# Kernel optimization log

Measured on AMD Instinct MI355X. Metric: run time of the kernel, lower is better.

Reference implementation:

```python
import jax, jax.numpy as jnp
import numpy as np

N_NODES = 100000
N_EDGES = 800000
D = 64      # conv_dim == out_dim (skip connection)
H = 128     # conv hidden width


def _w(k, i, o):
    return jax.random.normal(k, (i, o), jnp.float32) * (1.0 / np.sqrt(i))


def setup_inputs() -> dict:
    key = jax.random.key(0)
    ks = jax.random.split(key, 40)
    inp = {
        "edge_feat": jax.random.normal(ks[0], (N_EDGES, D), jnp.float32),
        "node_feat": jax.random.normal(ks[1], (N_NODES, D), jnp.float32),
        "graph_attr": jax.random.normal(ks[2], (1, D), jnp.float32),
        "src": jax.random.randint(ks[3], (N_EDGES,), 0, N_NODES),
        "dst": jax.random.randint(ks[4], (N_EDGES,), 0, N_NODES),
        # pre-dense MLPs (dims=[64,64], Softplus, activate_last)
        "pre_edge_w": _w(ks[5], D, D), "pre_edge_b": jnp.zeros((D,), jnp.float32),
        "pre_node_w": _w(ks[6], D, D), "pre_node_b": jnp.zeros((D,), jnp.float32),
        "pre_attr_w": _w(ks[7], D, D), "pre_attr_b": jnp.zeros((D,), jnp.float32),
        # conv edge MLP: [4D, H, H, D]
        "edge_w0": _w(ks[8], 4 * D, H), "edge_b0": jnp.zeros((H,), jnp.float32),
        "edge_w1": _w(ks[9], H, H),     "edge_b1": jnp.zeros((H,), jnp.float32),
        "edge_w2": _w(ks[10], H, D),    "edge_b2": jnp.zeros((D,), jnp.float32),
        # conv node MLP: [3D, H, H, D]
        "node_w0": _w(ks[11], 3 * D, H), "node_b0": jnp.zeros((H,), jnp.float32),
        "node_w1": _w(ks[12], H, H),     "node_b1": jnp.zeros((H,), jnp.float32),
        "node_w2": _w(ks[13], H, D),     "node_b2": jnp.zeros((D,), jnp.float32),
        # conv attr MLP: [3D, H, H, D]
        "attr_w0": _w(ks[14], 3 * D, H), "attr_b0": jnp.zeros((H,), jnp.float32),
        "attr_w1": _w(ks[15], H, H),     "attr_b1": jnp.zeros((H,), jnp.float32),
        "attr_w2": _w(ks[16], H, D),     "attr_b2": jnp.zeros((D,), jnp.float32),
    }
    return inp


def _mlp(x, layers):
    # Linear + Softplus after every layer (activate_last=True)
    for w, b in layers:
        x = jax.nn.softplus(x @ w + b)
    return x


def reference(edge_feat, node_feat, graph_attr, src, dst,
              pre_edge_w, pre_edge_b, pre_node_w, pre_node_b, pre_attr_w, pre_attr_b,
              edge_w0, edge_b0, edge_w1, edge_b1, edge_w2, edge_b2,
              node_w0, node_b0, node_w1, node_b1, node_w2, node_b2,
              attr_w0, attr_b0, attr_w1, attr_b1, attr_w2, attr_b2):
    e_in, v_in, u_in = edge_feat, node_feat, graph_attr

    # pre-dense MLPs
    e = _mlp(edge_feat, [(pre_edge_w, pre_edge_b)])   # [E, D]
    v = _mlp(node_feat, [(pre_node_w, pre_node_b)])   # [N, D]
    u = _mlp(graph_attr, [(pre_attr_w, pre_attr_b)])  # [1, D]

    n_nodes = v.shape[0]

    # edge update: hstack([v_src, v_dst, e, u_broadcast]) -> edge MLP
    edge_in = jnp.concatenate(
        [v[src], v[dst], e, jnp.broadcast_to(u, (e.shape[0], u.shape[1]))], axis=1)  # [E, 4D]
    e_new = _mlp(edge_in, [(edge_w0, edge_b0), (edge_w1, edge_b1), (edge_w2, edge_b2)])  # [E, D]

    # node update: mean of incoming edge messages (segment-mean over dst)
    cnt = jax.ops.segment_sum(jnp.ones((e_new.shape[0], 1), e_new.dtype), dst,
                              num_segments=n_nodes)
    ve = jax.ops.segment_sum(e_new, dst, num_segments=n_nodes) / jnp.maximum(cnt, 1.0)
    node_in = jnp.concatenate(
        [v, ve, jnp.broadcast_to(u, (n_nodes, u.shape[1]))], axis=1)  # [N, 3D]
    v_new = _mlp(node_in, [(node_w0, node_b0), (node_w1, node_b1), (node_w2, node_b2)])  # [N, D]

    # attr update: mean readouts over edges and nodes
    ue = jnp.mean(e_new, axis=0, keepdims=True)  # [1, D]
    uv = jnp.mean(v_new, axis=0, keepdims=True)  # [1, D]
    attr_in = jnp.concatenate([u, ue, uv], axis=1)  # [1, 3D]
    u_new = _mlp(attr_in, [(attr_w0, attr_b0), (attr_w1, attr_b1), (attr_w2, attr_b2)])  # [1, D]

    # skip connections
    return (e_new + e_in, v_new + v_in, u_new + u_in)
```

## Files before the change

### kernel.cpp

```cpp
#include <hip/hip_runtime.h>
#include <cstddef>


typedef __attribute__((ext_vector_type(8))) short short8;
typedef __attribute__((ext_vector_type(4))) float f32x4;
typedef __attribute__((ext_vector_type(4))) unsigned int u32x4;
typedef __attribute__((ext_vector_type(2))) unsigned int u32x2;

__device__ __forceinline__ float sp(float x) {
    return fmaxf(x, 0.f) + __logf(1.f + __expf(-fabsf(x)));
}
__device__ __forceinline__ unsigned short f2bf(float x) {
    unsigned int u = __float_as_uint(x);
    u += 0x7fff + ((u >> 16) & 1);
    return (unsigned short)(u >> 16);
}
__device__ __forceinline__ unsigned int cvtpk(float lo, float hi) {
    unsigned int r;
    asm("v_cvt_pk_bf16_f32 %0, %1, %2" : "=v"(r) : "v"(lo), "v"(hi));
    return r;
}
__device__ __forceinline__ u32x4 pack8(f32x4 a, f32x4 b) {
    u32x4 r;
    r.x = cvtpk(a[0], a[1]); r.y = cvtpk(a[2], a[3]);
    r.z = cvtpk(b[0], b[1]); r.w = cvtpk(b[2], b[3]);
    return r;
}
__device__ __forceinline__ float bflo(unsigned int u) { return __uint_as_float(u << 16); }
__device__ __forceinline__ float bfhi(unsigned int u) { return __uint_as_float(u & 0xffff0000u); }
__device__ __forceinline__ int swz(int row, int chunk, int stride) {
    return row * stride + 128 * (chunk >> 3) + 16 * ((chunk & 7) ^ (row & 7));
}
__device__ __forceinline__ f32x4 mfma16(short8 a, short8 b, f32x4 c) {
    return __builtin_amdgcn_mfma_f32_16x16x32_bf16(a, b, c, 0, 0, 0);
}

__global__ __launch_bounds__(256) void wprep(
    const float* __restrict__ Wpe, const float* __restrict__ We0,
    const float* __restrict__ We1, const float* __restrict__ We2,
    const float* __restrict__ Wn0, const float* __restrict__ Wn1,
    const float* __restrict__ Wn2, const float* __restrict__ Wpn,
    unsigned short* __restrict__ out)
{
    int idx = blockIdx.x * 256 + threadIdx.x;
    const float* src; int K, N, base;
    if      (idx < 4096)  { src = Wpe; K = 64;  N = 64;  base = 0; }
    else if (idx < 28672) { src = We0; K = 192; N = 128; base = 4096; }
    else if (idx < 45056) { src = We1; K = 128; N = 128; base = 28672; }
    else if (idx < 53248) { src = We2; K = 128; N = 64;  base = 45056; }
    else if (idx < 69632) { src = Wn0; K = 128; N = 128; base = 53248; }
    else if (idx < 86016) { src = Wn1; K = 128; N = 128; base = 69632; }
    else if (idx < 94208) { src = Wn2; K = 128; N = 64;  base = 86016; }
    else if (idx < 98304) { src = Wpn; K = 64;  N = 64;  base = 94208; }
    else return;
    int r = idx - base, n = r / K, k = r % K;
    out[idx] = f2bf(src[(size_t)k * N + n]);
}

__global__ __launch_bounds__(256) void pre_node_kernel(
    const float* __restrict__ nf, const unsigned short* __restrict__ WpnT,
    const float* __restrict__ b, unsigned short* __restrict__ vb, int N)
{
    __shared__ __align__(16) char lds[16384];
    const int t = threadIdx.x, w = t >> 6, l = t & 63;
    const int l15 = l & 15, l4 = l >> 4;
    const int n0 = blockIdx.x * 64;

#pragma unroll
    for (int rr = 0; rr < 2; ++rr) {
        int f = t + 256 * rr;
        int e = f >> 3, c = f & 7;
        int n = n0 + e; if (n >= N) n = N - 1;
        const float* p = nf + (size_t)n * 64 + c * 8;
        f32x4 x0 = *(const f32x4*)p, x1 = *(const f32x4*)(p + 4);
        *(u32x4*)(lds + swz(e, c, 128)) = pack8(x0, x1);
    }
    __syncthreads();
    {
        const int nr = w * 16;
        short8 A0 = *(const short8*)(WpnT + (nr + l15) * 64 + l4 * 8);
        short8 A1 = *(const short8*)(WpnT + (nr + l15) * 64 + 32 + l4 * 8);
        f32x4 bb = *(const f32x4*)(b + nr + l4 * 4);
        const int ochunk = (nr >> 3) + (l4 >> 1), obyte = (l4 & 1) * 8;
#pragma unroll
        for (int tt = 0; tt < 4; ++tt) {
            short8 b0 = *(const short8*)(lds + swz(tt * 16 + l15, l4, 128));
            short8 b1 = *(const short8*)(lds + swz(tt * 16 + l15, 4 + l4, 128));
            f32x4 acc = {0.f, 0.f, 0.f, 0.f};
            acc = mfma16(A0, b0, acc);
            acc = mfma16(A1, b1, acc);
            u32x2 p;
            p.x = cvtpk(sp(acc[0] + bb[0]), sp(acc[1] + bb[1]));
            p.y = cvtpk(sp(acc[2] + bb[2]), sp(acc[3] + bb[3]));
            *(u32x2*)(lds + 8192 + swz(tt * 16 + l15, ochunk, 128) + obyte) = p;
        }
    }
    __syncthreads();
#pragma unroll
    for (int rr = 0; rr < 2; ++rr) {
        int f = t + 256 * rr;
        int e = f >> 3, c = f & 7;
        int n = n0 + e;
        if (n < N) {
            u32x4 d = *(const u32x4*)(lds + 8192 + swz(e, c, 128));
            *(u32x4*)(vb + (size_t)n * 64 + c * 8) = d;
        }
    }
}

__global__ void pre_attr_kernel(
    const float* __restrict__ ga, const float* __restrict__ Wpa, const float* __restrict__ bpa,
    const float* __restrict__ eW0, const float* __restrict__ eb0,
    const float* __restrict__ nW0, const float* __restrict__ nb0,
    float* __restrict__ u, float* __restrict__ c0e, float* __restrict__ c0n)
{
    __shared__ float us[64];
    const int t = threadIdx.x;
    if (t < 64) {
        float acc = bpa[t];
        for (int k = 0; k < 64; ++k) acc += ga[k] * Wpa[k * 64 + t];
        float uu = sp(acc);
        us[t] = uu;
        u[t] = uu;
    }
    __syncthreads();
    if (t < 128) {
        float acc = eb0[t];
        for (int k = 0; k < 64; ++k) acc += us[k] * eW0[(192 + k) * 128 + t];
        c0e[t] = acc;
        float accn = nb0[t];
        for (int k = 0; k < 64; ++k) accn += us[k] * nW0[(128 + k) * 128 + t];
        c0n[t] = accn;
    }
}

__global__ __launch_bounds__(256) void cnt_kernel(
    const int* __restrict__ dst, int* __restrict__ cnt, int E)
{
    int i = blockIdx.x * 256 + threadIdx.x;
    if (i < E) atomicAdd(&cnt[dst[i]], 1);
}

__global__ __launch_bounds__(256) void scan1_kernel(
    const int* __restrict__ cnt, int* __restrict__ woff, int* __restrict__ bsum, int N)
{
    __shared__ int wsum[4];
    const int t = threadIdx.x, lane = t & 63, wv = t >> 6;
    const int i0 = blockIdx.x * 1024 + t * 4;
    int v0 = (i0 + 0 < N) ? cnt[i0 + 0] : 0;
    int v1 = (i0 + 1 < N) ? cnt[i0 + 1] : 0;
    int v2 = (i0 + 2 < N) ? cnt[i0 + 2] : 0;
    int v3 = (i0 + 3 < N) ? cnt[i0 + 3] : 0;
    int ts = v0 + v1 + v2 + v3;
    int sc = ts;
    for (int d = 1; d < 64; d <<= 1) {
        int up = __shfl_up(sc, d);
        if (lane >= d) sc += up;
    }
    if (lane == 63) wsum[wv] = sc;
    __syncthreads();
    int woffs = 0;
    for (int i = 0; i < wv; ++i) woffs += wsum[i];
    int ex = woffs + sc - ts;
    if (i0 + 0 < N) woff[i0 + 0] = ex;            ex += v0;
    if (i0 + 1 < N) woff[i0 + 1] = ex;            ex += v1;
    if (i0 + 2 < N) woff[i0 + 2] = ex;            ex += v2;
    if (i0 + 3 < N) woff[i0 + 3] = ex;
    if (t == 0) bsum[blockIdx.x] = wsum[0] + wsum[1] + wsum[2] + wsum[3];
}

__global__ void scan2_kernel(int* __restrict__ bsum, int nb)
{
    __shared__ int s[256];
    const int t = threadIdx.x;
    if (t < nb) s[t] = bsum[t];
    __syncthreads();
    if (t == 0) {
        int a = 0;
        for (int i = 0; i < nb; ++i) { int v = s[i]; s[i] = a; a += v; }
    }
    __syncthreads();
    if (t < nb) bsum[t] = s[t];
}

__global__ __launch_bounds__(256) void scan3_kernel(
    int* __restrict__ woff, int* __restrict__ wcur, const int* __restrict__ bsum, int N)
{
    const int base = blockIdx.x * 1024;
    const int add = bsum[blockIdx.x];
#pragma unroll
    for (int r = 0; r < 4; ++r) {
        int i = base + r * 256 + threadIdx.x;
        if (i < N) {
            int o = woff[i] + add;
            woff[i] = o;
            wcur[i] = o;
        }
    }
}

__global__ __launch_bounds__(256) void scatter_kernel(
    const int* __restrict__ dst, int* __restrict__ wcur, int* __restrict__ eidx, int E)
{
    int i = blockIdx.x * 256 + threadIdx.x;
    if (i < E) {
        int d = dst[i];
        int p = atomicAdd(&wcur[d], 1);
        eidx[p] = i;
    }
}

#define ELDS_X  0
#define ELDS_H  12288
#define ELDS_EF 12288

__global__ __launch_bounds__(256, 4) void edge_kernel(
    const float* __restrict__ ef, const unsigned short* __restrict__ vb,
    const int* __restrict__ src, const int* __restrict__ dst,
    const unsigned short* __restrict__ WpeT, const float* __restrict__ bpe,
    const unsigned short* __restrict__ W0T, const float* __restrict__ c0e,
    const unsigned short* __restrict__ W1T, const float* __restrict__ b1,
    const unsigned short* __restrict__ W2T, const float* __restrict__ b2,
    float* __restrict__ e_out, unsigned short* __restrict__ ebf)
{
    __shared__ __align__(16) char lds[20480];
    const int t = threadIdx.x;
    const int w = t >> 6, l = t & 63;
    const int l15 = l & 15, l4 = l >> 4;
    const int e0 = blockIdx.x * 32;

    f32x4 efr0, efr1;
    {
        int e = t >> 4, c = t & 15;
        efr0 = *(const f32x4*)(ef + (size_t)(e0 + e) * 64 + c * 4);
        u32x2 p;
        p.x = cvtpk(efr0[0], efr0[1]);
        p.y = cvtpk(efr0[2], efr0[3]);
        *(u32x2*)(lds + ELDS_EF + swz(e, c >> 1, 128) + (c & 1) * 8) = p;
        int f2 = t + 256;
        e = f2 >> 4; c = f2 & 15;
        efr1 = *(const f32x4*)(ef + (size_t)(e0 + e) * 64 + c * 4);
        p.x = cvtpk(efr1[0], efr1[1]);
        p.y = cvtpk(efr1[2], efr1[3]);
        *(u32x2*)(lds + ELDS_EF + swz(e, c >> 1, 128) + (c & 1) * 8) = p;
    }
#pragma unroll
    for (int rr = 0; rr < 2; ++rr) {
        int f = t + 256 * rr;
        int e = f >> 4, c = f & 15;
        int node = (c < 8) ? src[e0 + e] : dst[e0 + e];
        u32x4 d = *(const u32x4*)(vb + (size_t)node * 64 + (c & 7) * 8);
        *(u32x4*)(lds + ELDS_X + swz(e, c, 384)) = d;
    }
    __syncthreads();

    {
        const int nr = w * 16;
        short8 A0 = *(const short8*)(WpeT + (nr + l15) * 64 + l4 * 8);
        short8 A1 = *(const short8*)(WpeT + (nr + l15) * 64 + 32 + l4 * 8);
        f32x4 bb = *(const f32x4*)(bpe + nr + l4 * 4);
        const int ochunk = ((128 + nr) >> 3) + (l4 >> 1), obyte = (l4 & 1) * 8;
#pragma unroll
        for (int tt = 0; tt < 2; ++tt) {
            short8 b0 = *(const short8*)(lds + ELDS_EF + swz(tt * 16 + l15, l4, 128));
            short8 b1 = *(const short8*)(lds + ELDS_EF + swz(tt * 16 + l15, 4 + l4, 128));
            f32x4 acc = {0.f, 0.f, 0.f, 0.f};
            acc = mfma16(A0, b0, acc);
            acc = mfma16(A1, b1, acc);
            u32x2 p;
            p.x = cvtpk(sp(acc[0] + bb[0]), sp(acc[1] + bb[1]));
            p.y = cvtpk(sp(acc[2] + bb[2]), sp(acc[3] + bb[3]));
            *(u32x2*)(lds + ELDS_X + swz(tt * 16 + l15, ochunk, 384) + obyte) = p;
        }
    }
    __syncthreads();

    {
        const int nr0 = w * 32, nr1 = nr0 + 16;
        short8 A[2][6];
#pragma unroll
        for (int a = 0; a < 2; ++a)
#pragma unroll
            for (int ks = 0; ks < 6; ++ks)
                A[a][ks] = *(const short8*)(W0T + (nr0 + a * 16 + l15) * 192 + ks * 32 + l4 * 8);
        f32x4 bb0 = *(const f32x4*)(c0e + nr0 + l4 * 4);
        f32x4 bb1 = *(const f32x4*)(c0e + nr1 + l4 * 4);
        const int oc0 = (nr0 >> 3) + (l4 >> 1), oc1 = (nr1 >> 3) + (l4 >> 1);
        const int obyte = (l4 & 1) * 8;
#pragma unroll
        for (int tt = 0; tt < 2; ++tt) {
            f32x4 a0 = {0.f, 0.f, 0.f, 0.f}, a1 = {0.f, 0.f, 0.f, 0.f};
#pragma unroll
            for (int ks = 0; ks < 6; ++ks) {
                short8 b = *(const short8*)(lds + ELDS_X + swz(tt * 16 + l15, ks * 4 + l4, 384));
                a0 = mfma16(A[0][ks], b, a0);
                a1 = mfma16(A[1][ks], b, a1);
            }
            u32x2 p0, p1;
            p0.x = cvtpk(sp(a0[0] + bb0[0]), sp(a0[1] + bb0[1]));
            p0.y = cvtpk(sp(a0[2] + bb0[2]), sp(a0[3] + bb0[3]));
            p1.x = cvtpk(sp(a1[0] + bb1[0]), sp(a1[1] + bb1[1]));
            p1.y = cvtpk(sp(a1[2] + bb1[2]), sp(a1[3] + bb1[3]));
            *(u32x2*)(lds + ELDS_H + swz(tt * 16 + l15, oc0, 256) + obyte) = p0;
            *(u32x2*)(lds + ELDS_H + swz(tt * 16 + l15, oc1, 256) + obyte) = p1;
        }
    }
    __syncthreads();

    {
        const int nr0 = w * 32, nr1 = nr0 + 16;
        short8 A[2][4];
#pragma unroll
        for (int a = 0; a < 2; ++a)
#pragma unroll
            for (int ks = 0; ks < 4; ++ks)
                A[a][ks] = *(const short8*)(W1T + (nr0 + a * 16 + l15) * 128 + ks * 32 + l4 * 8);
        f32x4 bb0 = *(const f32x4*)(b1 + nr0 + l4 * 4);
        f32x4 bb1 = *(const f32x4*)(b1 + nr1 + l4 * 4);
        const int oc0 = (nr0 >> 3) + (l4 >> 1), oc1 = (nr1 >> 3) + (l4 >> 1);
        const int obyte = (l4 & 1) * 8;
#pragma unroll
        for (int tt = 0; tt < 2; ++tt) {
            f32x4 a0 = {0.f, 0.f, 0.f, 0.f}, a1 = {0.f, 0.f, 0.f, 0.f};
#pragma unroll
            for (int ks = 0; ks < 4; ++ks) {
                short8 b = *(const short8*)(lds + ELDS_H + swz(tt * 16 + l15, ks * 4 + l4, 256));
                a0 = mfma16(A[0][ks], b, a0);
                a1 = mfma16(A[1][ks], b, a1);
            }
            u32x2 p0, p1;
            p0.x = cvtpk(sp(a0[0] + bb0[0]), sp(a0[1] + bb0[1]));
            p0.y = cvtpk(sp(a0[2] + bb0[2]), sp(a0[3] + bb0[3]));
            p1.x = cvtpk(sp(a1[0] + bb1[0]), sp(a1[1] + bb1[1]));
            p1.y = cvtpk(sp(a1[2] + bb1[2]), sp(a1[3] + bb1[3]));
            *(u32x2*)(lds + ELDS_X + swz(tt * 16 + l15, oc0, 256) + obyte) = p0;
            *(u32x2*)(lds + ELDS_X + swz(tt * 16 + l15, oc1, 256) + obyte) = p1;
        }
    }
    __syncthreads();

    {
        const int nr = w * 16;
        short8 A[4];
#pragma unroll
        for (int ks = 0; ks < 4; ++ks)
            A[ks] = *(const short8*)(W2T + (nr + l15) * 128 + ks * 32 + l4 * 8);
        f32x4 bb = *(const f32x4*)(b2 + nr + l4 * 4);
        const int ochunk = (nr >> 2) + l4;
#pragma unroll
        for (int tt = 0; tt < 2; ++tt) {
            f32x4 acc = {0.f, 0.f, 0.f, 0.f};
#pragma unroll
            for (int ks = 0; ks < 4; ++ks) {
                short8 b = *(const short8*)(lds + ELDS_X + swz(tt * 16 + l15, ks * 4 + l4, 256));
                acc = mfma16(A[ks], b, acc);
            }
            f32x4 y = {sp(acc[0] + bb[0]), sp(acc[1] + bb[1]),
                       sp(acc[2] + bb[2]), sp(acc[3] + bb[3])};
            *(f32x4*)(lds + ELDS_H + swz(tt * 16 + l15, ochunk, 256)) = y;
        }
    }
    __syncthreads();

    {
        int e = t >> 4, c = t & 15;
        f32x4 en = *(const f32x4*)(lds + ELDS_H + swz(e, c, 256));
        *(f32x4*)(e_out + (size_t)(e0 + e) * 64 + c * 4) = en + efr0;
        if (ebf) {
            u32x2 pk;
            pk.x = cvtpk(en[0], en[1]);
            pk.y = cvtpk(en[2], en[3]);
            *(u32x2*)(ebf + (size_t)(e0 + e) * 64 + c * 4) = pk;
        }
        int f2 = t + 256;
        e = f2 >> 4; c = f2 & 15;
        en = *(const f32x4*)(lds + ELDS_H + swz(e, c, 256));
        *(f32x4*)(e_out + (size_t)(e0 + e) * 64 + c * 4) = en + efr1;
        if (ebf) {
            u32x2 pk;
            pk.x = cvtpk(en[0], en[1]);
            pk.y = cvtpk(en[2], en[3]);
            *(u32x2*)(ebf + (size_t)(e0 + e) * 64 + c * 4) = pk;
        }
    }
}

#define NLDS_X 0
#define NLDS_H 16384

__global__ __launch_bounds__(256, 3) void node_kernel(
    const float* __restrict__ nf, const unsigned short* __restrict__ vb,
    const int* __restrict__ cnt, const int* __restrict__ woff,
    const int* __restrict__ eidx,
    const unsigned short* __restrict__ ebf,
    const float* __restrict__ e_out_full, const float* __restrict__ ef_full,
    const unsigned short* __restrict__ W0T, const float* __restrict__ c0n,
    const unsigned short* __restrict__ W1T, const float* __restrict__ b1,
    const unsigned short* __restrict__ W2T, const float* __restrict__ b2,
    float* __restrict__ v_out, float* __restrict__ acc_e, float* __restrict__ acc_v,
    int N)
{
    __shared__ __align__(16) char lds[32768];
    const int t = threadIdx.x;
    const int w = t >> 6, l = t & 63;
    const int l15 = l & 15, l4 = l >> 4;
    const int n0 = blockIdx.x * 64;

#pragma unroll
    for (int rr = 0; rr < 2; ++rr) {
        int f = t + 256 * rr;
        int e = f >> 3, c = f & 7;
        int n = n0 + e; if (n >= N) n = N - 1;
        u32x4 d = *(const u32x4*)(vb + (size_t)n * 64 + c * 8);
        *(u32x4*)(lds + NLDS_X + swz(e, c, 256)) = d;
    }
    {
        const int e = t >> 2, p = t & 3;
        const int n = n0 + e;
        const bool valid = n < N;
        f32x4 a0 = {0,0,0,0}, a1 = {0,0,0,0}, a2 = {0,0,0,0}, a3 = {0,0,0,0};
        float rc = 0.f;
        if (valid) {
            const int off = woff[n], deg = cnt[n];
            rc = 1.f / fmaxf((float)deg, 1.f);
            if (ebf) {
                for (int j = 0; j < deg; ++j) {
                    int ed = eidx[off + j];
                    const unsigned short* row = ebf + (size_t)ed * 64 + p * 16;
                    u32x4 qa = *(const u32x4*)row;
                    u32x4 qb = *(const u32x4*)(row + 8);
                    a0[0] += bflo(qa.x); a0[1] += bfhi(qa.x);
                    a0[2] += bflo(qa.y); a0[3] += bfhi(qa.y);
                    a1[0] += bflo(qa.z); a1[1] += bfhi(qa.z);
                    a1[2] += bflo(qa.w); a1[3] += bfhi(qa.w);
                    a2[0] += bflo(qb.x); a2[1] += bfhi(qb.x);
                    a2[2] += bflo(qb.y); a2[3] += bfhi(qb.y);
                    a3[0] += bflo(qb.z); a3[1] += bfhi(qb.z);
                    a3[2] += bflo(qb.w); a3[3] += bfhi(qb.w);
                }
            } else {
                for (int j = 0; j < deg; ++j) {
                    int ed = eidx[off + j];
                    const float* ro = e_out_full + (size_t)ed * 64 + p * 16;
                    const float* ri = ef_full + (size_t)ed * 64 + p * 16;
                    a0 += *(const f32x4*)(ro + 0)  - *(const f32x4*)(ri + 0);
                    a1 += *(const f32x4*)(ro + 4)  - *(const f32x4*)(ri + 4);
                    a2 += *(const f32x4*)(ro + 8)  - *(const f32x4*)(ri + 8);
                    a3 += *(const f32x4*)(ro + 12) - *(const f32x4*)(ri + 12);
                }
            }
        }
        *(f32x4*)(lds + NLDS_H + swz(e, p * 4 + 0, 256)) = a0;
        *(f32x4*)(lds + NLDS_H + swz(e, p * 4 + 1, 256)) = a1;
        *(f32x4*)(lds + NLDS_H + swz(e, p * 4 + 2, 256)) = a2;
        *(f32x4*)(lds + NLDS_H + swz(e, p * 4 + 3, 256)) = a3;
        *(u32x4*)(lds + NLDS_X + swz(e, 8 + 2 * p, 256)) = pack8(a0 * rc, a1 * rc);
        *(u32x4*)(lds + NLDS_X + swz(e, 9 + 2 * p, 256)) = pack8(a2 * rc, a3 * rc);
    }
    __syncthreads();
    if (t < 64) {
        float s = 0.f;
        for (int row = 0; row < 64; ++row)
            s += *(const float*)(lds + NLDS_H + swz(row, t >> 2, 256) + (t & 3) * 4);
        atomicAdd(acc_e + t, s);
    }
    __syncthreads();

    {
        const int nr0 = w * 32, nr1 = nr0 + 16;
        short8 A[2][4];
#pragma unroll
        for (int a = 0; a < 2; ++a)
#pragma unroll
            for (int ks = 0; ks < 4; ++ks)
                A[a][ks] = *(const short8*)(W0T + (nr0 + a * 16 + l15) * 128 + ks * 32 + l4 * 8);
        f32x4 bb0 = *(const f32x4*)(c0n + nr0 + l4 * 4);
        f32x4 bb1 = *(const f32x4*)(c0n + nr1 + l4 * 4);
        const int oc0 = (nr0 >> 3) + (l4 >> 1), oc1 = (nr1 >> 3) + (l4 >> 1);
        const int obyte = (l4 & 1) * 8;
#pragma unroll
        for (int tt = 0; tt < 4; ++tt) {
            f32x4 a0 = {0.f, 0.f, 0.f, 0.f}, a1 = {0.f, 0.f, 0.f, 0.f};
#pragma unroll
            for (int ks = 0; ks < 4; ++ks) {
                short8 b = *(const short8*)(lds + NLDS_X + swz(tt * 16 + l15, ks * 4 + l4, 256));
                a0 = mfma16(A[0][ks], b, a0);
                a1 = mfma16(A[1][ks], b, a1);
            }
            u32x2 p0, p1;
            p0.x = cvtpk(sp(a0[0] + bb0[0]), sp(a0[1] + bb0[1]));
            p0.y = cvtpk(sp(a0[2] + bb0[2]), sp(a0[3] + bb0[3]));
            p1.x = cvtpk(sp(a1[0] + bb1[0]), sp(a1[1] + bb1[1]));
            p1.y = cvtpk(sp(a1[2] + bb1[2]), sp(a1[3] + bb1[3]));
            *(u32x2*)(lds + NLDS_H + swz(tt * 16 + l15, oc0, 256) + obyte) = p0;
            *(u32x2*)(lds + NLDS_H + swz(tt * 16 + l15, oc1, 256) + obyte) = p1;
        }
    }
    __syncthreads();

    {
        const int nr0 = w * 32, nr1 = nr0 + 16;
        short8 A[2][4];
#pragma unroll
        for (int a = 0; a < 2; ++a)
#pragma unroll
            for (int ks = 0; ks < 4; ++ks)
                A[a][ks] = *(const short8*)(W1T + (nr0 + a * 16 + l15) * 128 + ks * 32 + l4 * 8);
        f32x4 bb0 = *(const f32x4*)(b1 + nr0 + l4 * 4);
        f32x4 bb1 = *(const f32x4*)(b1 + nr1 + l4 * 4);
        const int oc0 = (nr0 >> 3) + (l4 >> 1), oc1 = (nr1 >> 3) + (l4 >> 1);
        const int obyte = (l4 & 1) * 8;
#pragma unroll
        for (int tt = 0; tt < 4; ++tt) {
            f32x4 a0 = {0.f, 0.f, 0.f, 0.f}, a1 = {0.f, 0.f, 0.f, 0.f};
#pragma unroll
            for (int ks = 0; ks < 4; ++ks) {
                short8 b = *(const short8*)(lds + NLDS_H + swz(tt * 16 + l15, ks * 4 + l4, 256));
                a0 = mfma16(A[0][ks], b, a0);
                a1 = mfma16(A[1][ks], b, a1);
            }
            u32x2 p0, p1;
            p0.x = cvtpk(sp(a0[0] + bb0[0]), sp(a0[1] + bb0[1]));
            p0.y = cvtpk(sp(a0[2] + bb0[2]), sp(a0[3] + bb0[3]));
            p1.x = cvtpk(sp(a1[0] + bb1[0]), sp(a1[1] + bb1[1]));
            p1.y = cvtpk(sp(a1[2] + bb1[2]), sp(a1[3] + bb1[3]));
            *(u32x2*)(lds + NLDS_X + swz(tt * 16 + l15, oc0, 256) + obyte) = p0;
            *(u32x2*)(lds + NLDS_X + swz(tt * 16 + l15, oc1, 256) + obyte) = p1;
        }
    }
    __syncthreads();

    {
        const int nr = w * 16;
        short8 A[4];
#pragma unroll
        for (int ks = 0; ks < 4; ++ks)
            A[ks] = *(const short8*)(W2T + (nr + l15) * 128 + ks * 32 + l4 * 8);
        f32x4 bb = *(const f32x4*)(b2 + nr + l4 * 4);
        const int ochunk = (nr >> 2) + l4;
#pragma unroll
        for (int tt = 0; tt < 4; ++tt) {
            f32x4 acc = {0.f, 0.f, 0.f, 0.f};
#pragma unroll
            for (int ks = 0; ks < 4; ++ks) {
                short8 b = *(const short8*)(lds + NLDS_X + swz(tt * 16 + l15, ks * 4 + l4, 256));
                acc = mfma16(A[ks], b, acc);
            }
            bool valid = (n0 + tt * 16 + l15) < N;
            f32x4 y;
            y[0] = valid ? sp(acc[0] + bb[0]) : 0.f;
            y[1] = valid ? sp(acc[1] + bb[1]) : 0.f;
            y[2] = valid ? sp(acc[2] + bb[2]) : 0.f;
            y[3] = valid ? sp(acc[3] + bb[3]) : 0.f;
            *(f32x4*)(lds + NLDS_H + swz(tt * 16 + l15, ochunk, 256)) = y;
        }
    }
    __syncthreads();

#pragma unroll
    for (int rr = 0; rr < 4; ++rr) {
        int f = t + 256 * rr;
        int e = f >> 4, c = f & 15;
        int n = n0 + e;
        if (n < N) {
            f32x4 vn = *(const f32x4*)(lds + NLDS_H + swz(e, c, 256));
            f32x4 x = *(const f32x4*)(nf + (size_t)n * 64 + c * 4);
            f32x4 o = vn + x;
            *(f32x4*)(v_out + (size_t)n * 64 + c * 4) = o;
        }
    }
    if (t < 64) {
        float s = 0.f;
        for (int row = 0; row < 64; ++row)
            s += *(const float*)(lds + NLDS_H + swz(row, t >> 2, 256) + (t & 3) * 4);
        atomicAdd(acc_v + t, s);
    }
}

__global__ void attr_kernel(
    const float* __restrict__ ga, const float* __restrict__ u,
    const float* __restrict__ acc_e, const float* __restrict__ acc_v,
    const float* __restrict__ W0, const float* __restrict__ b0,
    const float* __restrict__ W1, const float* __restrict__ b1,
    const float* __restrict__ W2, const float* __restrict__ b2,
    float* __restrict__ out_u, float Einv, float Ninv)
{
    __shared__ float ain[192];
    __shared__ float h0[128];
    __shared__ float h1[128];
    const int t = threadIdx.x;
    if (t < 64) {
        ain[t] = u[t];
        ain[64 + t] = acc_e[t] * Einv;
        ain[128 + t] = acc_v[t] * Ninv;
    }
    __syncthreads();
    if (t < 128) {
        float a = b0[t];
        for (int k = 0; k < 192; ++k) a += ain[k] * W0[k * 128 + t];
        h0[t] = sp(a);
    }
    __syncthreads();
    if (t < 128) {
        float a = b1[t];
        for (int k = 0; k < 128; ++k) a += h0[k] * W1[k * 128 + t];
        h1[t] = sp(a);
    }
    __syncthreads();
    if (t < 64) {
        float a = b2[t];
        for (int k = 0; k < 128; ++k) a += h1[k] * W2[k * 64 + t];
        out_u[t] = sp(a) + ga[t];
    }
}

extern "C" void kernel_launch(void* const* d_in, const int* in_sizes, int n_in,
                              void* d_out, int out_size, void* d_ws, size_t ws_size,
                              hipStream_t stream)
{
    const float* edge_feat = (const float*)d_in[0];
    const float* node_feat = (const float*)d_in[1];
    const float* graph_attr = (const float*)d_in[2];
    const int*   src = (const int*)d_in[3];
    const int*   dst = (const int*)d_in[4];
    const float* pre_edge_w = (const float*)d_in[5];
    const float* pre_edge_b = (const float*)d_in[6];
    const float* pre_node_w = (const float*)d_in[7];
    const float* pre_node_b = (const float*)d_in[8];
    const float* pre_attr_w = (const float*)d_in[9];
    const float* pre_attr_b = (const float*)d_in[10];
    const float* edge_w0 = (const float*)d_in[11];
    const float* edge_b0 = (const float*)d_in[12];
    const float* edge_w1 = (const float*)d_in[13];
    const float* edge_b1 = (const float*)d_in[14];
    const float* edge_w2 = (const float*)d_in[15];
    const float* edge_b2 = (const float*)d_in[16];
    const float* node_w0 = (const float*)d_in[17];
    const float* node_b0 = (const float*)d_in[18];
    const float* node_w1 = (const float*)d_in[19];
    const float* node_b1 = (const float*)d_in[20];
    const float* node_w2 = (const float*)d_in[21];
    const float* node_b2 = (const float*)d_in[22];
    const float* attr_w0 = (const float*)d_in[23];
    const float* attr_b0 = (const float*)d_in[24];
    const float* attr_w1 = (const float*)d_in[25];
    const float* attr_b1 = (const float*)d_in[26];
    const float* attr_w2 = (const float*)d_in[27];
    const float* attr_b2 = (const float*)d_in[28];

    const int E = in_sizes[0] / 64;
    const int N = in_sizes[1] / 64;
    const int NB = (N + 1023) / 1024;

    char* wsB = (char*)d_ws;
    size_t off = 0;
    auto alloc = [&](size_t bytes) { char* p = wsB + off; off += (bytes + 15) & ~(size_t)15; return p; };
    float* acc_e = (float*)alloc(64 * 4);
    float* acc_v = (float*)alloc(64 * 4);
    int*   cnt   = (int*)alloc((size_t)N * 4);
    float* u     = (float*)alloc(64 * 4);
    float* c0e   = (float*)alloc(128 * 4);
    float* c0n   = (float*)alloc(128 * 4);
    int*   bsum  = (int*)alloc((size_t)NB * 4);
    int*   woff  = (int*)alloc((size_t)N * 4);
    int*   wcur  = (int*)alloc((size_t)N * 4);
    int*   eidx  = (int*)alloc((size_t)E * 4);
    unsigned short* wT = (unsigned short*)alloc((size_t)98304 * 2);
    unsigned short* vb = (unsigned short*)alloc((size_t)N * 64 * 2);
    size_t off_no_ebf = off;
    unsigned short* ebf = (unsigned short*)alloc((size_t)E * 64 * 2);
    const bool use_ebf = (off <= ws_size);
    if (!use_ebf) { ebf = nullptr; off = off_no_ebf; }

    unsigned short* WpeT = wT;
    unsigned short* We0T = wT + 4096;
    unsigned short* We1T = wT + 28672;
    unsigned short* We2T = wT + 45056;
    unsigned short* Wn0T = wT + 53248;
    unsigned short* Wn1T = wT + 69632;
    unsigned short* Wn2T = wT + 86016;
    unsigned short* WpnT = wT + 94208;

    float* e_out = (float*)d_out;
    float* v_out = e_out + (size_t)E * 64;
    float* u_out = v_out + (size_t)N * 64;

    hipMemsetAsync(acc_e, 0, (size_t)(128 + N) * 4, stream);

    wprep<<<384, 256, 0, stream>>>(pre_edge_w, edge_w0, edge_w1, edge_w2,
                                   node_w0, node_w1, node_w2, pre_node_w, wT);
    pre_node_kernel<<<(N + 63) / 64, 256, 0, stream>>>(node_feat, WpnT, pre_node_b, vb, N);
    pre_attr_kernel<<<1, 128, 0, stream>>>(graph_attr, pre_attr_w, pre_attr_b,
                                           edge_w0, edge_b0, node_w0, node_b0,
                                           u, c0e, c0n);
    cnt_kernel<<<(E + 255) / 256, 256, 0, stream>>>(dst, cnt, E);
    scan1_kernel<<<NB, 256, 0, stream>>>(cnt, woff, bsum, N);
    scan2_kernel<<<1, 256, 0, stream>>>(bsum, NB);
    scan3_kernel<<<NB, 256, 0, stream>>>(woff, wcur, bsum, N);
    scatter_kernel<<<(E + 255) / 256, 256, 0, stream>>>(dst, wcur, eidx, E);
    edge_kernel<<<E / 32, 256, 0, stream>>>(
        edge_feat, vb, src, dst,
        WpeT, pre_edge_b, We0T, c0e, We1T, edge_b1, We2T, edge_b2,
        e_out, ebf);
    node_kernel<<<(N + 63) / 64, 256, 0, stream>>>(
        node_feat, vb, cnt, woff, eidx, ebf, e_out, edge_feat,
        Wn0T, c0n, Wn1T, node_b1, Wn2T, node_b2,
        v_out, acc_e, acc_v, N);
    attr_kernel<<<1, 128, 0, stream>>>(
        graph_attr, u, acc_e, acc_v,
        attr_w0, attr_b0, attr_w1, attr_b1, attr_w2, attr_b2,
        u_out, 1.f / (float)E, 1.f / (float)N);
}
```

Before: 625.3 us.

## Write edge messages in dst-sorted order, hoist edge weights, fuse count into wprep

```diff
diff --git a/kernel.cpp b/kernel.cpp
--- a/kernel.cpp
+++ b/kernel.cpp
@@ -40,9 +40,12 @@
     const float* __restrict__ We1, const float* __restrict__ We2,
     const float* __restrict__ Wn0, const float* __restrict__ Wn1,
     const float* __restrict__ Wn2, const float* __restrict__ Wpn,
-    unsigned short* __restrict__ out)
+    unsigned short* __restrict__ out,
+    const int* __restrict__ dst, int* __restrict__ cnt, int E)
 {
     int idx = blockIdx.x * 256 + threadIdx.x;
+    for (int i = idx; i < E; i += 384 * 256) atomicAdd(&cnt[dst[i]], 1);
+
     const float* src; int K, N, base;
     if      (idx < 4096)  { src = Wpe; K = 64;  N = 64;  base = 0; }
     else if (idx < 28672) { src = We0; K = 192; N = 128; base = 4096; }
@@ -134,13 +137,6 @@
     }
 }
 
-__global__ __launch_bounds__(256) void cnt_kernel(
-    const int* __restrict__ dst, int* __restrict__ cnt, int E)
-{
-    int i = blockIdx.x * 256 + threadIdx.x;
-    if (i < E) atomicAdd(&cnt[dst[i]], 1);
-}
-
 __global__ __launch_bounds__(256) void scan1_kernel(
     const int* __restrict__ cnt, int* __restrict__ woff, int* __restrict__ bsum, int N)
 {
@@ -200,13 +196,15 @@
 }
 
 __global__ __launch_bounds__(256) void scatter_kernel(
-    const int* __restrict__ dst, int* __restrict__ wcur, int* __restrict__ eidx, int E)
+    const int* __restrict__ dst, int* __restrict__ wcur,
+    int* __restrict__ eidx, int* __restrict__ slot, int E)
 {
     int i = blockIdx.x * 256 + threadIdx.x;
     if (i < E) {
         int d = dst[i];
         int p = atomicAdd(&wcur[d], 1);
         eidx[p] = i;
+        slot[i] = p;
     }
 }
 
@@ -214,9 +212,10 @@
 #define ELDS_H  12288
 #define ELDS_EF 12288
 
-__global__ __launch_bounds__(256, 4) void edge_kernel(
+__global__ __launch_bounds__(256, 3) void edge_kernel(
     const float* __restrict__ ef, const unsigned short* __restrict__ vb,
     const int* __restrict__ src, const int* __restrict__ dst,
+    const int* __restrict__ slot,
     const unsigned short* __restrict__ WpeT, const float* __restrict__ bpe,
     const unsigned short* __restrict__ W0T, const float* __restrict__ c0e,
     const unsigned short* __restrict__ W1T, const float* __restrict__ b1,
@@ -229,9 +228,30 @@
     const int l15 = l & 15, l4 = l >> 4;
     const int e0 = blockIdx.x * 32;
 
+    const int nrS = w * 16;
+    const int nr0 = w * 32, nr1 = nr0 + 16;
+    short8 Wp[2], W0f[2][6], W1f[2][4], W2f[4];
+    Wp[0] = *(const short8*)(WpeT + (nrS + l15) * 64 + l4 * 8);
+    Wp[1] = *(const short8*)(WpeT + (nrS + l15) * 64 + 32 + l4 * 8);
+#pragma unroll
+    for (int a = 0; a < 2; ++a)
+#pragma unroll
+        for (int ks = 0; ks < 6; ++ks)
+            W0f[a][ks] = *(const short8*)(W0T + (nr0 + a * 16 + l15) * 192 + ks * 32 + l4 * 8);
+#pragma unroll
+    for (int a = 0; a < 2; ++a)
+#pragma unroll
+        for (int ks = 0; ks < 4; ++ks)
+            W1f[a][ks] = *(const short8*)(W1T + (nr0 + a * 16 + l15) * 128 + ks * 32 + l4 * 8);
+#pragma unroll
+    for (int ks = 0; ks < 4; ++ks)
+        W2f[ks] = *(const short8*)(W2T + (nrS + l15) * 128 + ks * 32 + l4 * 8);
+
     f32x4 efr0, efr1;
+    int sl0, sl1;
     {
         int e = t >> 4, c = t & 15;
+        sl0 = slot[e0 + e];
         efr0 = *(const f32x4*)(ef + (size_t)(e0 + e) * 64 + c * 4);
         u32x2 p;
         p.x = cvtpk(efr0[0], efr0[1]);
@@ -239,6 +259,7 @@
         *(u32x2*)(lds + ELDS_EF + swz(e, c >> 1, 128) + (c & 1) * 8) = p;
         int f2 = t + 256;
         e = f2 >> 4; c = f2 & 15;
+        sl1 = slot[e0 + e];
         efr1 = *(const f32x4*)(ef + (size_t)(e0 + e) * 64 + c * 4);
         p.x = cvtpk(efr1[0], efr1[1]);
         p.y = cvtpk(efr1[2], efr1[3]);
@@ -255,18 +276,15 @@
     __syncthreads();
 
     {
-        const int nr = w * 16;
-        short8 A0 = *(const short8*)(WpeT + (nr + l15) * 64 + l4 * 8);
-        short8 A1 = *(const short8*)(WpeT + (nr + l15) * 64 + 32 + l4 * 8);
-        f32x4 bb = *(const f32x4*)(bpe + nr + l4 * 4);
-        const int ochunk = ((128 + nr) >> 3) + (l4 >> 1), obyte = (l4 & 1) * 8;
+        f32x4 bb = *(const f32x4*)(bpe + nrS + l4 * 4);
+        const int ochunk = ((128 + nrS) >> 3) + (l4 >> 1), obyte = (l4 & 1) * 8;
 #pragma unroll
         for (int tt = 0; tt < 2; ++tt) {
             short8 b0 = *(const short8*)(lds + ELDS_EF + swz(tt * 16 + l15, l4, 128));
             short8 b1 = *(const short8*)(lds + ELDS_EF + swz(tt * 16 + l15, 4 + l4, 128));
             f32x4 acc = {0.f, 0.f, 0.f, 0.f};
-            acc = mfma16(A0, b0, acc);
-            acc = mfma16(A1, b1, acc);
+            acc = mfma16(Wp[0], b0, acc);
+            acc = mfma16(Wp[1], b1, acc);
             u32x2 p;
             p.x = cvtpk(sp(acc[0] + bb[0]), sp(acc[1] + bb[1]));
             p.y = cvtpk(sp(acc[2] + bb[2]), sp(acc[3] + bb[3]));
@@ -276,13 +294,6 @@
     __syncthreads();
 
     {
-        const int nr0 = w * 32, nr1 = nr0 + 16;
-        short8 A[2][6];
-#pragma unroll
-        for (int a = 0; a < 2; ++a)
-#pragma unroll
-            for (int ks = 0; ks < 6; ++ks)
-                A[a][ks] = *(const short8*)(W0T + (nr0 + a * 16 + l15) * 192 + ks * 32 + l4 * 8);
         f32x4 bb0 = *(const f32x4*)(c0e + nr0 + l4 * 4);
         f32x4 bb1 = *(const f32x4*)(c0e + nr1 + l4 * 4);
         const int oc0 = (nr0 >> 3) + (l4 >> 1), oc1 = (nr1 >> 3) + (l4 >> 1);
@@ -293,8 +304,8 @@
 #pragma unroll
             for (int ks = 0; ks < 6; ++ks) {
                 short8 b = *(const short8*)(lds + ELDS_X + swz(tt * 16 + l15, ks * 4 + l4, 384));
-                a0 = mfma16(A[0][ks], b, a0);
-                a1 = mfma16(A[1][ks], b, a1);
+                a0 = mfma16(W0f[0][ks], b, a0);
+                a1 = mfma16(W0f[1][ks], b, a1);
             }
             u32x2 p0, p1;
             p0.x = cvtpk(sp(a0[0] + bb0[0]), sp(a0[1] + bb0[1]));
@@ -308,13 +319,6 @@
     __syncthreads();
 
     {
-        const int nr0 = w * 32, nr1 = nr0 + 16;
-        short8 A[2][4];
-#pragma unroll
-        for (int a = 0; a < 2; ++a)
-#pragma unroll
-            for (int ks = 0; ks < 4; ++ks)
-                A[a][ks] = *(const short8*)(W1T + (nr0 + a * 16 + l15) * 128 + ks * 32 + l4 * 8);
         f32x4 bb0 = *(const f32x4*)(b1 + nr0 + l4 * 4);
         f32x4 bb1 = *(const f32x4*)(b1 + nr1 + l4 * 4);
         const int oc0 = (nr0 >> 3) + (l4 >> 1), oc1 = (nr1 >> 3) + (l4 >> 1);
@@ -325,8 +329,8 @@
 #pragma unroll
             for (int ks = 0; ks < 4; ++ks) {
                 short8 b = *(const short8*)(lds + ELDS_H + swz(tt * 16 + l15, ks * 4 + l4, 256));
-                a0 = mfma16(A[0][ks], b, a0);
-                a1 = mfma16(A[1][ks], b, a1);
+                a0 = mfma16(W1f[0][ks], b, a0);
+                a1 = mfma16(W1f[1][ks], b, a1);
             }
             u32x2 p0, p1;
             p0.x = cvtpk(sp(a0[0] + bb0[0]), sp(a0[1] + bb0[1]));
@@ -340,20 +344,15 @@
     __syncthreads();
 
     {
-        const int nr = w * 16;
-        short8 A[4];
-#pragma unroll
-        for (int ks = 0; ks < 4; ++ks)
-            A[ks] = *(const short8*)(W2T + (nr + l15) * 128 + ks * 32 + l4 * 8);
-        f32x4 bb = *(const f32x4*)(b2 + nr + l4 * 4);
-        const int ochunk = (nr >> 2) + l4;
+        f32x4 bb = *(const f32x4*)(b2 + nrS + l4 * 4);
+        const int ochunk = (nrS >> 2) + l4;
 #pragma unroll
         for (int tt = 0; tt < 2; ++tt) {
             f32x4 acc = {0.f, 0.f, 0.f, 0.f};
 #pragma unroll
             for (int ks = 0; ks < 4; ++ks) {
                 short8 b = *(const short8*)(lds + ELDS_X + swz(tt * 16 + l15, ks * 4 + l4, 256));
-                acc = mfma16(A[ks], b, acc);
+                acc = mfma16(W2f[ks], b, acc);
             }
             f32x4 y = {sp(acc[0] + bb[0]), sp(acc[1] + bb[1]),
                        sp(acc[2] + bb[2]), sp(acc[3] + bb[3])};
@@ -370,7 +369,7 @@
             u32x2 pk;
             pk.x = cvtpk(en[0], en[1]);
             pk.y = cvtpk(en[2], en[3]);
-            *(u32x2*)(ebf + (size_t)(e0 + e) * 64 + c * 4) = pk;
+            *(u32x2*)(ebf + (size_t)sl0 * 64 + c * 4) = pk;
         }
         int f2 = t + 256;
         e = f2 >> 4; c = f2 & 15;
@@ -380,7 +379,7 @@
             u32x2 pk;
             pk.x = cvtpk(en[0], en[1]);
             pk.y = cvtpk(en[2], en[3]);
-            *(u32x2*)(ebf + (size_t)(e0 + e) * 64 + c * 4) = pk;
+            *(u32x2*)(ebf + (size_t)sl1 * 64 + c * 4) = pk;
         }
     }
 }
@@ -424,11 +423,11 @@
             const int off = woff[n], deg = cnt[n];
             rc = 1.f / fmaxf((float)deg, 1.f);
             if (ebf) {
+                const unsigned short* base = ebf + (size_t)off * 64 + p * 16;
                 for (int j = 0; j < deg; ++j) {
-                    int ed = eidx[off + j];
-                    const unsigned short* row = ebf + (size_t)ed * 64 + p * 16;
-                    u32x4 qa = *(const u32x4*)row;
-                    u32x4 qb = *(const u32x4*)(row + 8);
+                    u32x4 qa = *(const u32x4*)(base);
+                    u32x4 qb = *(const u32x4*)(base + 8);
+                    base += 64;
                     a0[0] += bflo(qa.x); a0[1] += bfhi(qa.x);
                     a0[2] += bflo(qa.y); a0[3] += bfhi(qa.y);
                     a1[0] += bflo(qa.z); a1[1] += bfhi(qa.z);
@@ -665,6 +664,7 @@
     int*   woff  = (int*)alloc((size_t)N * 4);
     int*   wcur  = (int*)alloc((size_t)N * 4);
     int*   eidx  = (int*)alloc((size_t)E * 4);
+    int*   slot  = (int*)alloc((size_t)E * 4);
     unsigned short* wT = (unsigned short*)alloc((size_t)98304 * 2);
     unsigned short* vb = (unsigned short*)alloc((size_t)N * 64 * 2);
     size_t off_no_ebf = off;
@@ -688,18 +688,18 @@
     hipMemsetAsync(acc_e, 0, (size_t)(128 + N) * 4, stream);
 
     wprep<<<384, 256, 0, stream>>>(pre_edge_w, edge_w0, edge_w1, edge_w2,
-                                   node_w0, node_w1, node_w2, pre_node_w, wT);
+                                   node_w0, node_w1, node_w2, pre_node_w, wT,
+                                   dst, cnt, E);
     pre_node_kernel<<<(N + 63) / 64, 256, 0, stream>>>(node_feat, WpnT, pre_node_b, vb, N);
     pre_attr_kernel<<<1, 128, 0, stream>>>(graph_attr, pre_attr_w, pre_attr_b,
                                            edge_w0, edge_b0, node_w0, node_b0,
                                            u, c0e, c0n);
-    cnt_kernel<<<(E + 255) / 256, 256, 0, stream>>>(dst, cnt, E);
     scan1_kernel<<<NB, 256, 0, stream>>>(cnt, woff, bsum, N);
     scan2_kernel<<<1, 256, 0, stream>>>(bsum, NB);
     scan3_kernel<<<NB, 256, 0, stream>>>(woff, wcur, bsum, N);
-    scatter_kernel<<<(E + 255) / 256, 256, 0, stream>>>(dst, wcur, eidx, E);
+    scatter_kernel<<<(E + 255) / 256, 256, 0, stream>>>(dst, wcur, eidx, slot, E);
     edge_kernel<<<E / 32, 256, 0, stream>>>(
-        edge_feat, vb, src, dst,
+        edge_feat, vb, src, dst, slot,
         WpeT, pre_edge_b, We0T, c0e, We1T, edge_b1, We2T, edge_b2,
         e_out, ebf);
     node_kernel<<<(N + 63) / 64, 256, 0, stream>>>(
```

After: 628.0 us. Within noise of the previous version (+0.4%).
